# Optimization experiments

Measured on AMD Instinct MI355X. Metric: run time of the kernel, lower is better.

The kernel has to match this reference:

```python
import jax, jax.numpy as jnp
import numpy as np
from jax import lax

EPS = 1e-10
ALPHA = 1000.0

def _gauss_kernel(k=3, mu=0.0, sigma=3.0):
    g1 = np.linspace(-1.0, 1.0, k)
    x, y = np.meshgrid(g1, g1)
    d = np.sqrt(x ** 2 + y ** 2)
    g = np.exp(-(d - mu) ** 2 / (2.0 * sigma ** 2)) / (2.0 * np.pi * sigma ** 2)
    return jnp.asarray(g / g.sum(), jnp.float32)

def _sobel_kernel(k=3, transpose=False):
    r = np.linspace(-(k // 2), k // 2, k)
    x, y = np.meshgrid(r, r)
    den = x ** 2 + y ** 2
    den[:, k // 2] = 1.0
    s = x / den
    if transpose:
        s = s.T
    return jnp.asarray(s, jnp.float32)

def _canny_nms_kernels():
    # 8 directional difference kernels (center minus neighbor), E, SE, S, SW, W, NW, N, NE
    off = [(1, 2), (2, 2), (2, 1), (2, 0), (1, 0), (0, 0), (0, 1), (0, 2)]
    k = np.zeros((8, 3, 3), np.float32)
    k[:, 1, 1] = 1.0
    for i, (r, c) in enumerate(off):
        k[i, r, c] = -1.0
    return jnp.asarray(k)

def _dwconv_reflect(x, k2d):
    # depthwise 3x3 conv with reflect padding (same as padding_mode='reflect', groups=C)
    C = x.shape[1]
    xp = jnp.pad(x, ((0, 0), (0, 0), (1, 1), (1, 1)), mode='reflect')
    w = jnp.broadcast_to(k2d[None, None], (C, 1, 3, 3))
    return lax.conv_general_dilated(xp, w, (1, 1), 'VALID', feature_group_count=C)

def _forward(x, w_expand, w_perm_gauss, w_perm_sx, w_perm_sy, w_merge, low_t, high_t):
    gauss = _gauss_kernel(3, 0.0, 3.0)
    sob_x = _sobel_kernel(3, transpose=False)
    sob_y = _sobel_kernel(3, transpose=True)
    canny = _canny_nms_kernels()  # (8,3,3)
    # 1x1 channel expansion
    h = jnp.einsum('oc,bchw->bohw', w_expand, x)
    # gaussian blur (depthwise) + trainable 1x1 permute
    g = jnp.einsum('oc,bchw->bohw', w_perm_gauss, _dwconv_reflect(h, gauss))
    gx = jnp.einsum('oc,bchw->bohw', w_perm_sx, _dwconv_reflect(g, sob_x))
    gy = jnp.einsum('oc,bchw->bohw', w_perm_sy, _dwconv_reflect(g, sob_y))
    mag = jnp.sqrt(gx * gx + gy * gy + EPS)  # (B,C,H,W)
    # NMSConv2d: every output kernel applies the same directional diff summed over ALL input
    # channels, so the 8C outputs repeat with period 8 -> compute 8 dirs on the channel-sum.
    s = jnp.sum(mag, axis=1, keepdims=True)  # (B,1,H,W)
    dirs = lax.conv_general_dilated(s, canny[:, None], (1, 1), [(1, 1), (1, 1)])  # (B,8,H,W)
    deg = jnp.arctan2(gy, gx) * (180.0 / np.pi)
    idx = jnp.mod(jnp.round(deg / 45.0), 8.0).astype(jnp.int32)  # (B,C,H,W) in [0,8)
    pos = jnp.take_along_axis(dirs[:, None], idx[:, :, None], axis=2)[:, :, 0]
    neg = jnp.take_along_axis(dirs[:, None], ((idx + 4) % 8)[:, :, None], axis=2)[:, :, 0]
    nms = mag * ((pos > 0) & (neg > 0)).astype(mag.dtype)
    # soft double threshold (steep sigmoids)
    strong = jax.nn.sigmoid(ALPHA * (nms - high_t))
    weak = 0.5 * (jax.nn.sigmoid(ALPHA * (high_t - nms)) - jax.nn.sigmoid(ALPHA * (low_t - nms)))
    thr = weak + strong
    # merge C -> 1
    m = jnp.einsum('oc,bchw->bohw', w_merge, thr)  # (B,1,H,W)
    # one-step hysteresis: strong pixels promote neighbouring weak (==0.5) pixels
    img_strong = jnp.where(m == 1.0, m, 0.0)
    masked = (m == 0.5)
    hyst = _dwconv_reflect(img_strong, jnp.full((3, 3), 1.25, m.dtype))
    changed = jnp.where((hyst > 1.0) & masked, m, 0.0) + img_strong
    return changed

def setup_inputs() -> dict:
    key = jax.random.key(0)
    k0, k1, k2 = jax.random.split(key, 3)
    B, Cin, C, H, W = 8, 3, 8, 512, 512
    x = jax.random.uniform(k0, (B, Cin, H, W), jnp.float32)
    w_expand = jax.nn.softmax(jax.random.uniform(k1, (C, Cin), jnp.float32), axis=0)
    eye = jnp.eye(C, dtype=jnp.float32)
    bound = 1.0 / np.sqrt(C)
    w_merge = jax.random.uniform(k2, (1, C), jnp.float32, minval=-bound, maxval=bound)
    low_t = jnp.full((C, 1, 1), 0.1, jnp.float32)
    high_t = jnp.full((C, 1, 1), 0.2, jnp.float32)
    return {'x': x, 'w_expand': w_expand, 'w_perm_gauss': eye, 'w_perm_sx': eye,
            'w_perm_sy': eye, 'w_merge': w_merge, 'low_t': low_t, 'high_t': high_t}

def reference(x, w_expand, w_perm_gauss, w_perm_sx, w_perm_sy, w_merge, low_t, high_t):
    return _forward(x, w_expand, w_perm_gauss, w_perm_sx, w_perm_sy, w_merge, low_t, high_t)
```

## Files before the change

kernel.cpp:

```cpp
#include <hip/hip_runtime.h>
#include <math.h>

#define Bsz 8
#define HWp (512*512)
#define TS 32
#define SG 36
#define MG 34
#define XW 40
#define BW 38
#define NT 512
#define K2E 1442.6950408889634f
#define T2q 0.17157287525380993f

typedef float f2 __attribute__((ext_vector_type(2)));

#if __has_builtin(__builtin_amdgcn_exp2f)
#define EXP2F(x) __builtin_amdgcn_exp2f(x)
#else
#define EXP2F(x) __expf(0.6931471805599453f*(x))
#endif

__device__ __forceinline__ int refl(int i, int n) {
    i = (i < 0) ? -i : i;
    return (i >= n) ? (2*n - 2 - i) : i;
}

__global__ void k_mats(const float* __restrict__ we, const float* __restrict__ pg,
                       const float* __restrict__ psx, const float* __restrict__ psy,
                       const float* __restrict__ wm, const float* __restrict__ lowt,
                       const float* __restrict__ hight, float* __restrict__ mats) {
    if (threadIdx.x == 0 && blockIdx.x == 0) {
        float M1[8][3];
        for (int o = 0; o < 8; ++o)
            for (int c = 0; c < 3; ++c) {
                float a = 0.f;
                for (int k = 0; k < 8; ++k) a += pg[o*8+k] * we[k*3+c];
                M1[o][c] = a;
            }
        for (int o = 0; o < 8; ++o)
            for (int c = 0; c < 3; ++c) {
                float a = 0.f, b = 0.f;
                for (int k = 0; k < 8; ++k) { a += psx[o*8+k]*M1[k][c]; b += psy[o*8+k]*M1[k][c]; }
                mats[o*3+c]      = a;
                mats[24 + o*3+c] = b;
            }
        for (int o = 0; o < 8; ++o) {
            mats[48+o] = hight[o] * K2E;
            mats[56+o] = lowt[o]  * K2E;
            mats[64+o] = 0.5f * wm[o];
        }
        for (int j = 0; j < 4; ++j)
            for (int k = 0; k < 3; ++k)
                for (int e = 0; e < 2; ++e) {
                    mats[72  + (j*3+k)*2 + e] = mats[(2*j+e)*3 + k];
                    mats[120 + (j*3+k)*2 + e] = mats[24 + (2*j+e)*3 + k];
                }
    }
}

__global__ __launch_bounds__(NT) void k_fused(
    const float* __restrict__ x, const float* __restrict__ mats,
    float* __restrict__ out, float wc, float wE, float wk)
{
    __shared__ float sm1[3*XW*XW];
    __shared__ float blb[3*BW*BW];
    __shared__ int anyS;

    const int b  = blockIdx.z;
    const int x0 = blockIdx.x*TS, y0 = blockIdx.y*TS;
    const int t  = threadIdx.x;
    const bool inter = (blockIdx.x > 0) && ((int)blockIdx.x < (int)gridDim.x-1) &&
                       (blockIdx.y > 0) && ((int)blockIdx.y < (int)gridDim.y-1);

    if (t == 0) anyS = 0;

    const float* xb = x + (size_t)b*3*HWp;

    if (inter) {
        const float* xo = xb + (size_t)(y0-4)*512 + (x0-4);
        for (int i = t; i < 3*XW*10; i += NT) {
            int c = i/400; int j = i - c*400; int r = j/10; int q = j - r*10;
            float4 v = *(const float4*)(xo + (size_t)c*HWp + r*512 + q*4);
            *(float4*)&sm1[c*(XW*XW) + r*XW + q*4] = v;
        }
    } else {
        for (int i = t; i < XW*XW; i += NT) {
            int r = i/XW, cc = i - r*XW;
            size_t off = (size_t)refl(y0-4+r,512)*512 + refl(x0-4+cc,512);
            #pragma unroll
            for (int c = 0; c < 3; ++c)
                sm1[c*(XW*XW)+i] = xb[(size_t)c*HWp + off];
        }
    }
    __syncthreads();

    if (inter) {
        if (t < 494) {
            int g = t/38, cb = t - g*38, r0 = 3*g;
            #pragma unroll
            for (int c = 0; c < 3; ++c) {
                const float* col = &sm1[c*(XW*XW) + cb];
                float* bo = &blb[c*(BW*BW) + cb];
                float a0 = col[r0*XW],     a1 = col[r0*XW+1],     a2 = col[r0*XW+2];
                float e0 = col[(r0+1)*XW], e1 = col[(r0+1)*XW+1], e2 = col[(r0+1)*XW+2];
                #pragma unroll
                for (int ir = 0; ir < 3; ++ir) {
                    int r = r0 + ir;
                    if (r < BW) {
                        float f0 = col[(r+2)*XW], f1 = col[(r+2)*XW+1], f2v = col[(r+2)*XW+2];
                        float t0 = a0+f0, t1 = a1+f1, t2 = a2+f2v;
                        float u = t0+t2, v = e0+e2, w = t1+v;
                        bo[r*BW] = wk*u + wE*w + wc*e1;
                        a0=e0; a1=e1; a2=e2; e0=f0; e1=f1; e2=f2v;
                    }
                }
            }
        }
    } else {
        for (int i = t; i < BW*BW; i += NT) {
            int r = i/BW, cc = i - r*BW;
            int iy = refl(y0-3+r,512) - (y0-4);
            int ix = refl(x0-3+cc,512) - (x0-4);
            const int base = iy*XW + ix;
            #pragma unroll
            for (int c = 0; c < 3; ++c) {
                const float* xp = &sm1[c*(XW*XW) + base];
                blb[c*(BW*BW)+i] =
                    wk*(xp[-XW-1]+xp[-XW+1]+xp[XW-1]+xp[XW+1]) +
                    wE*(xp[-XW]+xp[-1]+xp[1]+xp[XW]) + wc*xp[0];
            }
        }
    }
    __syncthreads();

    float mg[3][8];
    unsigned qk[3];
    const int gC = t/36, csC = t - gC*36, r0C = 3*gC;
    const bool actC = (t < 432);
    if (actC) {
        float txv[3][3], tyv[3][3];
        #pragma unroll
        for (int c = 0; c < 3; ++c) {
            const float* blc = &blb[c*(BW*BW) + csC];
            float p0 = blc[r0C*BW],     p1 = blc[r0C*BW+1],     p2 = blc[r0C*BW+2];
            float q0 = blc[(r0C+1)*BW], q1 = blc[(r0C+1)*BW+1], q2 = blc[(r0C+1)*BW+2];
            float D0 = p2-p0, E0 = fmaf(0.5f, p0+p2, p1);
            float D1 = q2-q0, E1 = fmaf(0.5f, q0+q2, q1);
            #pragma unroll
            for (int ir = 0; ir < 3; ++ir) {
                const float* wr = &blc[(r0C+2+ir)*BW];
                float w0 = wr[0], w1 = wr[1], w2 = wr[2];
                float D2 = w2-w0, E2 = fmaf(0.5f, w0+w2, w1);
                txv[ir][c] = fmaf(0.5f, D0+D2, D1);
                tyv[ir][c] = E2 - E0;
                D0 = D1; D1 = D2; E0 = E1; E1 = E2;
            }
        }
        const f2* A2 = (const f2*)(mats + 72);
        const f2* B2 = (const f2*)(mats + 120);
        #pragma unroll
        for (int ir = 0; ir < 3; ++ir) {
            f2 s2 = {0.f, 0.f};
            unsigned pk = 0;
            #pragma unroll
            for (int j = 0; j < 4; ++j) {
                f2 gx = A2[j*3+0]*txv[ir][0] + A2[j*3+1]*txv[ir][1] + A2[j*3+2]*txv[ir][2];
                f2 gy = B2[j*3+0]*tyv[ir][0] + B2[j*3+1]*tyv[ir][1] + B2[j*3+2]*tyv[ir][2];
                f2 gx2 = gx*gx, gy2 = gy*gy;
                f2 r2 = gx2 + gy2 + (f2){1e-10f, 1e-10f};
                float m0 = __builtin_amdgcn_sqrtf(r2.x);
                float m1 = __builtin_amdgcn_sqrtf(r2.y);
                mg[ir][2*j] = m0; mg[ir][2*j+1] = m1;
                s2 += (f2){m0, m1};
                unsigned d0 = 1u | (((__float_as_uint(gx.x) ^ __float_as_uint(gy.x)) >> 30) & 2u);
                unsigned q0 = (gx2.x <= T2q*gy2.x) ? 2u : d0;
                q0 = (gy2.x <= T2q*gx2.x) ? 0u : q0;
                unsigned d1 = 1u | (((__float_as_uint(gx.y) ^ __float_as_uint(gy.y)) >> 30) & 2u);
                unsigned q1 = (gx2.y <= T2q*gy2.y) ? 2u : d1;
                q1 = (gy2.y <= T2q*gx2.y) ? 0u : q1;
                pk |= (q0 << (4*j)) | (q1 << (4*j+2));
            }
            qk[ir] = pk;
            #pragma unroll
            for (int o = 0; o < 8; ++o) { asm volatile("" : "+v"(mg[ir][o])); }
            asm volatile("" : "+v"(qk[ir]));
            int rr = r0C + ir;
            int gy_ = y0-2+rr, gx_ = x0-2+csC;
            bool inimg = ((unsigned)gy_ < 512u) && ((unsigned)gx_ < 512u);
            sm1[rr*SG + csC] = inimg ? (s2.x + s2.y) : 0.f;
        }
    }
    __syncthreads();

    bool anyL = false;
    {
        const float* sS = sm1;
        float* mS = sm1 + SG*SG;
        const f2* hiK2 = (const f2*)(mats + 48);
        const f2* loK2 = (const f2*)(mats + 56);
        const f2* wm2  = (const f2*)(mats + 64);
        if (actC && csC >= 1 && csC <= 34) {
            int ra = r0C-1 < 0 ? 0 : r0C-1;
            int rb = r0C;
            int rc = r0C+1;
            const float* pa = &sS[ra*SG + csC];
            const float* pb = &sS[rb*SG + csC];
            const float* pc = &sS[rc*SG + csC];
            float l0=pa[-1], c0=pa[0], r0v=pa[1];
            float l1=pb[-1], c1=pb[0], r1v=pb[1];
            float l2=pc[-1], c2=pc[0], r2v=pc[1];
            #pragma unroll
            for (int ir = 0; ir < 3; ++ir) {
                int r = r0C + ir;
                if (r >= 1 && r <= 34) {
                    float sc = c1;
                    unsigned mask = 0;
                    mask |= ((sc > r1v) && (sc > l1)) ? 1u : 0u;
                    mask |= ((sc > r2v) && (sc > l0)) ? 2u : 0u;
                    mask |= ((sc > c2)  && (sc > c0)) ? 4u : 0u;
                    mask |= ((sc > l2)  && (sc > r0v)) ? 8u : 0u;
                    unsigned pk = qk[ir];
                    f2 acc = {0.f, 0.f};
                    #pragma unroll
                    for (int j = 0; j < 4; ++j) {
                        unsigned ii = pk >> (4*j);
                        f2 nms;
                        nms.x = ((mask >> (ii & 3u)) & 1u)      ? mg[ir][2*j]   : 0.f;
                        nms.y = ((mask >> ((ii>>2) & 3u)) & 1u) ? mg[ir][2*j+1] : 0.f;
                        f2 aH = nms * (f2){-K2E,-K2E} + hiK2[j];
                        f2 aL = nms * (f2){-K2E,-K2E} + loK2[j];
                        f2 sh = { __builtin_amdgcn_rcpf(1.f + EXP2F(aH.x)),
                                  __builtin_amdgcn_rcpf(1.f + EXP2F(aH.y)) };
                        f2 sl = { __builtin_amdgcn_rcpf(1.f + EXP2F(aL.x)),
                                  __builtin_amdgcn_rcpf(1.f + EXP2F(aL.y)) };
                        acc += wm2[j]*(sh + sl);
                    }
                    float m = acc.x + acc.y;
                    mS[(r-1)*MG + (csC-1)] = m;
                    anyL |= (m == 1.0f);
                }
                if (ir < 2) {
                    int rn = r0C + 2 + ir; rn = rn > 35 ? 35 : rn;
                    const float* pn = &sS[rn*SG + csC];
                    l0=l1; c0=c1; r0v=r1v;
                    l1=l2; c1=c2; r1v=r2v;
                    l2=pn[-1]; c2=pn[0]; r2v=pn[1];
                }
            }
        }
    }
    if (anyL) anyS = 1;
    __syncthreads();

    {
        const float* mS = sm1 + SG*SG;
        float* op = out + (size_t)b*HWp;
        if (anyS == 0) {
            if (t < 256) {
                int row = t >> 3, q = t & 7;
                float4 z = {0.f, 0.f, 0.f, 0.f};
                *(float4*)(op + (size_t)(y0+row)*512 + x0 + q*4) = z;
            }
        } else {
            for (int i2 = t; i2 < TS*TS; i2 += NT) {
                int ty_ = i2>>5, tx_ = i2&31;
                int y = y0 + ty_, xg = x0 + tx_;
                const float* mp = &mS[(ty_+1)*MG + (tx_+1)];
                float mc = mp[0];
                float hy = 0.f;
                if (inter) {
                    #pragma unroll
                    for (int dy = -1; dy <= 1; ++dy)
                        #pragma unroll
                        for (int dx = -1; dx <= 1; ++dx)
                            hy += (mp[dy*MG+dx] == 1.0f) ? 1.25f : 0.f;
                } else {
                    #pragma unroll
                    for (int dy = -1; dy <= 1; ++dy)
                        #pragma unroll
                        for (int dx = -1; dx <= 1; ++dx) {
                            int ly = refl(y+dy,512) - (y0-1);
                            int lx = refl(xg+dx,512) - (x0-1);
                            hy += (mS[ly*MG+lx] == 1.0f) ? 1.25f : 0.f;
                        }
                }
                float strong = (mc == 1.0f) ? mc : 0.f;
                op[(size_t)y*512 + xg] =
                    (((hy > 1.0f) && (mc == 0.5f)) ? mc : 0.f) + strong;
            }
        }
    }
}

extern "C" void kernel_launch(void* const* d_in, const int* in_sizes, int n_in,
                              void* d_out, int out_size, void* d_ws, size_t ws_size,
                              hipStream_t stream) {
    const float* x    = (const float*)d_in[0];
    const float* we   = (const float*)d_in[1];
    const float* pg   = (const float*)d_in[2];
    const float* psx  = (const float*)d_in[3];
    const float* psy  = (const float*)d_in[4];
    const float* wm   = (const float*)d_in[5];
    const float* lowt = (const float*)d_in[6];
    const float* hit  = (const float*)d_in[7];
    float* mats = (float*)d_ws;
    float* outp = (float*)d_out;

    double e1 = exp(-1.0/18.0), e2 = exp(-2.0/18.0);
    double sum = 1.0 + 4.0*e1 + 4.0*e2;
    float wc = (float)(1.0/sum), wE = (float)(e1/sum), wk = (float)(e2/sum);

    k_mats<<<1, 64, 0, stream>>>(we, pg, psx, psy, wm, lowt, hit, mats);
    k_fused<<<dim3(512/TS, 512/TS, Bsz), dim3(NT), 0, stream>>>(
        x, mats, outp, wc, wE, wk);
}
```

Measured before the change: 52.17 us.

## Widen tiles to 64x32 with 1024 threads and fold weight prep into fused kernel

Changes the tile from 32x32 to 64x32 with 1024 threads per block, which shrinks the relative halo overhead for loads and the blur/gradient stages. Removes the separate single-thread k_mats launch. Each block now computes the combined channel matrices in shared memory and reads them as wave-uniform values via readfirstlane. Larger blocks and more shared memory per block may lower occupancy, and every block redoes the small matrix computation.

```diff
diff --git a/kernel.cpp b/kernel.cpp
--- a/kernel.cpp
+++ b/kernel.cpp
@@ -3,12 +3,17 @@
 
 #define Bsz 8
 #define HWp (512*512)
-#define TS 32
-#define SG 36
-#define MG 34
-#define XW 40
-#define BW 38
-#define NT 512
+#define TSX 64
+#define TSY 32
+#define XR 40
+#define XC 72
+#define BR 38
+#define BC 70
+#define SR 36
+#define SC 68
+#define MR 34
+#define MC 66
+#define NT 1024
 #define K2E 1442.6950408889634f
 #define T2q 0.17157287525380993f
 
@@ -24,154 +29,170 @@
     i = (i < 0) ? -i : i;
     return (i >= n) ? (2*n - 2 - i) : i;
 }
-
-__global__ void k_mats(const float* __restrict__ we, const float* __restrict__ pg,
-                       const float* __restrict__ psx, const float* __restrict__ psy,
-                       const float* __restrict__ wm, const float* __restrict__ lowt,
-                       const float* __restrict__ hight, float* __restrict__ mats) {
-    if (threadIdx.x == 0 && blockIdx.x == 0) {
-        float M1[8][3];
-        for (int o = 0; o < 8; ++o)
-            for (int c = 0; c < 3; ++c) {
-                float a = 0.f;
-                for (int k = 0; k < 8; ++k) a += pg[o*8+k] * we[k*3+c];
-                M1[o][c] = a;
-            }
-        for (int o = 0; o < 8; ++o)
-            for (int c = 0; c < 3; ++c) {
-                float a = 0.f, b = 0.f;
-                for (int k = 0; k < 8; ++k) { a += psx[o*8+k]*M1[k][c]; b += psy[o*8+k]*M1[k][c]; }
-                mats[o*3+c]      = a;
-                mats[24 + o*3+c] = b;
-            }
-        for (int o = 0; o < 8; ++o) {
-            mats[48+o] = hight[o] * K2E;
-            mats[56+o] = lowt[o]  * K2E;
-            mats[64+o] = 0.5f * wm[o];
-        }
-        for (int j = 0; j < 4; ++j)
-            for (int k = 0; k < 3; ++k)
-                for (int e = 0; e < 2; ++e) {
-                    mats[72  + (j*3+k)*2 + e] = mats[(2*j+e)*3 + k];
-                    mats[120 + (j*3+k)*2 + e] = mats[24 + (2*j+e)*3 + k];
-                }
-    }
-}
-
-__global__ __launch_bounds__(NT) void k_fused(
-    const float* __restrict__ x, const float* __restrict__ mats,
+__device__ __forceinline__ float ldsUf(float v) {
+    return __uint_as_float(__builtin_amdgcn_readfirstlane(__float_as_uint(v)));
+}
+__device__ __forceinline__ f2 ldsU2(const float* p) {
+    f2 v = *(const f2*)p;
+    f2 r; r.x = ldsUf(v.x); r.y = ldsUf(v.y);
+    return r;
+}
+__device__ __forceinline__ f2 splat(float v) { f2 r = {v, v}; return r; }
+
+__global__ __launch_bounds__(NT, 4) void k_fused(
+    const float* __restrict__ x,
+    const float* __restrict__ we, const float* __restrict__ pg,
+    const float* __restrict__ psx, const float* __restrict__ psy,
+    const float* __restrict__ wm, const float* __restrict__ lowt,
+    const float* __restrict__ hight,
     float* __restrict__ out, float wc, float wE, float wk)
 {
-    __shared__ float sm1[3*XW*XW];
-    __shared__ float blb[3*BW*BW];
+    __shared__ __align__(16) float xw[3*XR*XC];
+    __shared__ __align__(16) float blb[3*BR*BC];
+    __shared__ __align__(16) float matsL[168];
     __shared__ int anyS;
 
     const int b  = blockIdx.z;
-    const int x0 = blockIdx.x*TS, y0 = blockIdx.y*TS;
+    const int x0 = blockIdx.x*TSX, y0 = blockIdx.y*TSY;
     const int t  = threadIdx.x;
     const bool inter = (blockIdx.x > 0) && ((int)blockIdx.x < (int)gridDim.x-1) &&
                        (blockIdx.y > 0) && ((int)blockIdx.y < (int)gridDim.y-1);
 
     if (t == 0) anyS = 0;
 
+    if (t < 24) {
+        int o = t/3, c = t - o*3;
+        float a = 0.f;
+        #pragma unroll
+        for (int k = 0; k < 8; ++k) a = fmaf(pg[o*8+k], we[k*3+c], a);
+        matsL[144 + t] = a;
+        float av = 0.f, bv = 0.f;
+        #pragma unroll
+        for (int k = 0; k < 8; ++k) {
+            float m1 = matsL[144 + k*3 + c];
+            av = fmaf(psx[o*8+k], m1, av);
+            bv = fmaf(psy[o*8+k], m1, bv);
+        }
+        matsL[t]      = av;
+        matsL[24 + t] = bv;
+        int pi = ((o>>1)*3 + c)*2 + (o&1);
+        matsL[72  + pi] = av;
+        matsL[120 + pi] = bv;
+    } else if (t < 32) {
+        int o = t - 24;
+        matsL[48+o] = hight[o] * K2E;
+        matsL[56+o] = lowt[o]  * K2E;
+        matsL[64+o] = 0.5f * wm[o];
+    }
+
     const float* xb = x + (size_t)b*3*HWp;
 
     if (inter) {
         const float* xo = xb + (size_t)(y0-4)*512 + (x0-4);
-        for (int i = t; i < 3*XW*10; i += NT) {
-            int c = i/400; int j = i - c*400; int r = j/10; int q = j - r*10;
+        for (int i = t; i < 3*XR*18; i += NT) {
+            int c = i/720; int j = i - c*720; int r = j/18; int q = j - r*18;
             float4 v = *(const float4*)(xo + (size_t)c*HWp + r*512 + q*4);
-            *(float4*)&sm1[c*(XW*XW) + r*XW + q*4] = v;
+            *(float4*)&xw[c*(XR*XC) + r*XC + q*4] = v;
         }
     } else {
-        for (int i = t; i < XW*XW; i += NT) {
-            int r = i/XW, cc = i - r*XW;
+        for (int i = t; i < XR*XC; i += NT) {
+            int r = i/XC, cc = i - r*XC;
             size_t off = (size_t)refl(y0-4+r,512)*512 + refl(x0-4+cc,512);
             #pragma unroll
             for (int c = 0; c < 3; ++c)
-                sm1[c*(XW*XW)+i] = xb[(size_t)c*HWp + off];
+                xw[c*(XR*XC)+i] = xb[(size_t)c*HWp + off];
         }
     }
     __syncthreads();
 
     if (inter) {
-        if (t < 494) {
-            int g = t/38, cb = t - g*38, r0 = 3*g;
+        if (t < 13*BC) {
+            int g = t/BC, cb = t - g*BC, r0 = 3*g;
             #pragma unroll
             for (int c = 0; c < 3; ++c) {
-                const float* col = &sm1[c*(XW*XW) + cb];
-                float* bo = &blb[c*(BW*BW) + cb];
-                float a0 = col[r0*XW],     a1 = col[r0*XW+1],     a2 = col[r0*XW+2];
-                float e0 = col[(r0+1)*XW], e1 = col[(r0+1)*XW+1], e2 = col[(r0+1)*XW+2];
+                const float* col = &xw[c*(XR*XC) + cb];
+                float* bo = &blb[c*(BR*BC) + cb];
+                float a0 = col[r0*XC],     a1 = col[r0*XC+1],     a2 = col[r0*XC+2];
+                float e0 = col[(r0+1)*XC], e1 = col[(r0+1)*XC+1], e2 = col[(r0+1)*XC+2];
                 #pragma unroll
                 for (int ir = 0; ir < 3; ++ir) {
                     int r = r0 + ir;
-                    if (r < BW) {
-                        float f0 = col[(r+2)*XW], f1 = col[(r+2)*XW+1], f2v = col[(r+2)*XW+2];
+                    if (r < BR) {
+                        float f0 = col[(r+2)*XC], f1 = col[(r+2)*XC+1], f2v = col[(r+2)*XC+2];
                         float t0 = a0+f0, t1 = a1+f1, t2 = a2+f2v;
                         float u = t0+t2, v = e0+e2, w = t1+v;
-                        bo[r*BW] = wk*u + wE*w + wc*e1;
+                        bo[r*BC] = wk*u + wE*w + wc*e1;
                         a0=e0; a1=e1; a2=e2; e0=f0; e1=f1; e2=f2v;
                     }
                 }
             }
         }
     } else {
-        for (int i = t; i < BW*BW; i += NT) {
-            int r = i/BW, cc = i - r*BW;
+        for (int i = t; i < BR*BC; i += NT) {
+            int r = i/BC, cc = i - r*BC;
             int iy = refl(y0-3+r,512) - (y0-4);
             int ix = refl(x0-3+cc,512) - (x0-4);
-            const int base = iy*XW + ix;
+            const int base = iy*XC + ix;
             #pragma unroll
             for (int c = 0; c < 3; ++c) {
-                const float* xp = &sm1[c*(XW*XW) + base];
-                blb[c*(BW*BW)+i] =
-                    wk*(xp[-XW-1]+xp[-XW+1]+xp[XW-1]+xp[XW+1]) +
-                    wE*(xp[-XW]+xp[-1]+xp[1]+xp[XW]) + wc*xp[0];
+                const float* xp = &xw[c*(XR*XC) + base];
+                blb[c*(BR*BC)+i] =
+                    wk*(xp[-XC-1]+xp[-XC+1]+xp[XC-1]+xp[XC+1]) +
+                    wE*(xp[-XC]+xp[-1]+xp[1]+xp[XC]) + wc*xp[0];
             }
         }
     }
     __syncthreads();
 
-    float mg[3][8];
+    f2 mg2[3][4];
     unsigned qk[3];
-    const int gC = t/36, csC = t - gC*36, r0C = 3*gC;
-    const bool actC = (t < 432);
+    const int gC = t/SC, csC = t - gC*SC, r0C = 3*gC;
+    const bool actC = (t < 12*SC);
     if (actC) {
-        float txv[3][3], tyv[3][3];
+        f2 A2[12], B2[12];
+        #pragma unroll
+        for (int j = 0; j < 12; ++j) {
+            A2[j] = ldsU2(matsL + 72  + 2*j);
+            B2[j] = ldsU2(matsL + 120 + 2*j);
+        }
+        float D0[3], D1[3], E0[3], E1[3];
         #pragma unroll
         for (int c = 0; c < 3; ++c) {
-            const float* blc = &blb[c*(BW*BW) + csC];
-            float p0 = blc[r0C*BW],     p1 = blc[r0C*BW+1],     p2 = blc[r0C*BW+2];
-            float q0 = blc[(r0C+1)*BW], q1 = blc[(r0C+1)*BW+1], q2 = blc[(r0C+1)*BW+2];
-            float D0 = p2-p0, E0 = fmaf(0.5f, p0+p2, p1);
-            float D1 = q2-q0, E1 = fmaf(0.5f, q0+q2, q1);
-            #pragma unroll
-            for (int ir = 0; ir < 3; ++ir) {
-                const float* wr = &blc[(r0C+2+ir)*BW];
+            const float* blc = &blb[c*(BR*BC) + csC];
+            float p0 = blc[r0C*BC],     p1 = blc[r0C*BC+1],     p2 = blc[r0C*BC+2];
+            float q0 = blc[(r0C+1)*BC], q1 = blc[(r0C+1)*BC+1], q2 = blc[(r0C+1)*BC+2];
+            D0[c] = p2-p0; E0[c] = fmaf(0.5f, p0+p2, p1);
+            D1[c] = q2-q0; E1[c] = fmaf(0.5f, q0+q2, q1);
+        }
+        const f2 eps2 = {1e-10f, 1e-10f};
+        #pragma unroll
+        for (int ir = 0; ir < 3; ++ir) {
+            float txv[3], tyv[3];
+            #pragma unroll
+            for (int c = 0; c < 3; ++c) {
+                const float* wr = &blb[c*(BR*BC) + (r0C+2+ir)*BC + csC];
                 float w0 = wr[0], w1 = wr[1], w2 = wr[2];
                 float D2 = w2-w0, E2 = fmaf(0.5f, w0+w2, w1);
-                txv[ir][c] = fmaf(0.5f, D0+D2, D1);
-                tyv[ir][c] = E2 - E0;
-                D0 = D1; D1 = D2; E0 = E1; E1 = E2;
-            }
-        }
-        const f2* A2 = (const f2*)(mats + 72);
-        const f2* B2 = (const f2*)(mats + 120);
-        #pragma unroll
-        for (int ir = 0; ir < 3; ++ir) {
+                txv[c] = fmaf(0.5f, D0[c]+D2, D1[c]);
+                tyv[c] = E2 - E0[c];
+                D0[c] = D1[c]; D1[c] = D2; E0[c] = E1[c]; E1[c] = E2;
+            }
             f2 s2 = {0.f, 0.f};
             unsigned pk = 0;
             #pragma unroll
             for (int j = 0; j < 4; ++j) {
-                f2 gx = A2[j*3+0]*txv[ir][0] + A2[j*3+1]*txv[ir][1] + A2[j*3+2]*txv[ir][2];
-                f2 gy = B2[j*3+0]*tyv[ir][0] + B2[j*3+1]*tyv[ir][1] + B2[j*3+2]*tyv[ir][2];
+                f2 gx = __builtin_elementwise_fma(A2[j*3+0], splat(txv[0]),
+                        __builtin_elementwise_fma(A2[j*3+1], splat(txv[1]),
+                                                  A2[j*3+2]*splat(txv[2])));
+                f2 gy = __builtin_elementwise_fma(B2[j*3+0], splat(tyv[0]),
+                        __builtin_elementwise_fma(B2[j*3+1], splat(tyv[1]),
+                                                  B2[j*3+2]*splat(tyv[2])));
                 f2 gx2 = gx*gx, gy2 = gy*gy;
-                f2 r2 = gx2 + gy2 + (f2){1e-10f, 1e-10f};
-                float m0 = __builtin_amdgcn_sqrtf(r2.x);
-                float m1 = __builtin_amdgcn_sqrtf(r2.y);
-                mg[ir][2*j] = m0; mg[ir][2*j+1] = m1;
-                s2 += (f2){m0, m1};
+                f2 r2 = gx2 + gy2 + eps2;
+                f2 m; m.x = __builtin_amdgcn_sqrtf(r2.x);
+                      m.y = __builtin_amdgcn_sqrtf(r2.y);
+                mg2[ir][j] = m;
+                s2 += m;
                 unsigned d0 = 1u | (((__float_as_uint(gx.x) ^ __float_as_uint(gy.x)) >> 30) & 2u);
                 unsigned q0 = (gx2.x <= T2q*gy2.x) ? 2u : d0;
                 q0 = (gy2.x <= T2q*gx2.x) ? 0u : q0;
@@ -182,37 +203,40 @@
             }
             qk[ir] = pk;
             #pragma unroll
-            for (int o = 0; o < 8; ++o) { asm volatile("" : "+v"(mg[ir][o])); }
+            for (int j = 0; j < 4; ++j) { asm volatile("" : "+v"(mg2[ir][j])); }
             asm volatile("" : "+v"(qk[ir]));
             int rr = r0C + ir;
             int gy_ = y0-2+rr, gx_ = x0-2+csC;
             bool inimg = ((unsigned)gy_ < 512u) && ((unsigned)gx_ < 512u);
-            sm1[rr*SG + csC] = inimg ? (s2.x + s2.y) : 0.f;
+            xw[rr*SC + csC] = inimg ? (s2.x + s2.y) : 0.f;
         }
     }
     __syncthreads();
 
     bool anyL = false;
     {
-        const float* sS = sm1;
-        float* mS = sm1 + SG*SG;
-        const f2* hiK2 = (const f2*)(mats + 48);
-        const f2* loK2 = (const f2*)(mats + 56);
-        const f2* wm2  = (const f2*)(mats + 64);
-        if (actC && csC >= 1 && csC <= 34) {
+        const float* sS = xw;
+        float* mS = xw + SR*SC;
+        if (actC && csC >= 1 && csC <= MC) {
+            f2 hiK2[4], loK2[4], wm2[4];
+            #pragma unroll
+            for (int j = 0; j < 4; ++j) {
+                hiK2[j] = ldsU2(matsL + 48 + 2*j);
+                loK2[j] = ldsU2(matsL + 56 + 2*j);
+                wm2[j]  = ldsU2(matsL + 64 + 2*j);
+            }
             int ra = r0C-1 < 0 ? 0 : r0C-1;
-            int rb = r0C;
-            int rc = r0C+1;
-            const float* pa = &sS[ra*SG + csC];
-            const float* pb = &sS[rb*SG + csC];
-            const float* pc = &sS[rc*SG + csC];
+            const float* pa = &sS[ra*SC + csC];
+            const float* pb = &sS[r0C*SC + csC];
+            const float* pc = &sS[(r0C+1)*SC + csC];
             float l0=pa[-1], c0=pa[0], r0v=pa[1];
             float l1=pb[-1], c1=pb[0], r1v=pb[1];
             float l2=pc[-1], c2=pc[0], r2v=pc[1];
+            const f2 nK2E = {-K2E, -K2E};
             #pragma unroll
             for (int ir = 0; ir < 3; ++ir) {
                 int r = r0C + ir;
-                if (r >= 1 && r <= 34) {
+                if (r >= 1 && r <= MR) {
                     float sc = c1;
                     unsigned mask = 0;
                     mask |= ((sc > r1v) && (sc > l1)) ? 1u : 0u;
@@ -225,23 +249,23 @@
                     for (int j = 0; j < 4; ++j) {
                         unsigned ii = pk >> (4*j);
                         f2 nms;
-                        nms.x = ((mask >> (ii & 3u)) & 1u)      ? mg[ir][2*j]   : 0.f;
-                        nms.y = ((mask >> ((ii>>2) & 3u)) & 1u) ? mg[ir][2*j+1] : 0.f;
-                        f2 aH = nms * (f2){-K2E,-K2E} + hiK2[j];
-                        f2 aL = nms * (f2){-K2E,-K2E} + loK2[j];
-                        f2 sh = { __builtin_amdgcn_rcpf(1.f + EXP2F(aH.x)),
-                                  __builtin_amdgcn_rcpf(1.f + EXP2F(aH.y)) };
-                        f2 sl = { __builtin_amdgcn_rcpf(1.f + EXP2F(aL.x)),
-                                  __builtin_amdgcn_rcpf(1.f + EXP2F(aL.y)) };
-                        acc += wm2[j]*(sh + sl);
+                        nms.x = ((mask >> (ii & 3u)) & 1u)      ? mg2[ir][j].x : 0.f;
+                        nms.y = ((mask >> ((ii>>2) & 3u)) & 1u) ? mg2[ir][j].y : 0.f;
+                        f2 aH = __builtin_elementwise_fma(nms, nK2E, hiK2[j]);
+                        f2 aL = __builtin_elementwise_fma(nms, nK2E, loK2[j]);
+                        f2 sh; sh.x = __builtin_amdgcn_rcpf(1.f + EXP2F(aH.x));
+                               sh.y = __builtin_amdgcn_rcpf(1.f + EXP2F(aH.y));
+                        f2 sl; sl.x = __builtin_amdgcn_rcpf(1.f + EXP2F(aL.x));
+                               sl.y = __builtin_amdgcn_rcpf(1.f + EXP2F(aL.y));
+                        acc = __builtin_elementwise_fma(wm2[j], sh + sl, acc);
                     }
                     float m = acc.x + acc.y;
-                    mS[(r-1)*MG + (csC-1)] = m;
+                    mS[(r-1)*MC + (csC-1)] = m;
                     anyL |= (m == 1.0f);
                 }
                 if (ir < 2) {
-                    int rn = r0C + 2 + ir; rn = rn > 35 ? 35 : rn;
-                    const float* pn = &sS[rn*SG + csC];
+                    int rn = r0C + 2 + ir; rn = rn > SR-1 ? SR-1 : rn;
+                    const float* pn = &sS[rn*SC + csC];
                     l0=l1; c0=c1; r0v=r1v;
                     l1=l2; c1=c2; r1v=r2v;
                     l2=pn[-1]; c2=pn[0]; r2v=pn[1];
@@ -253,19 +277,19 @@
     __syncthreads();
 
     {
-        const float* mS = sm1 + SG*SG;
+        const float* mS = xw + SR*SC;
         float* op = out + (size_t)b*HWp;
         if (anyS == 0) {
-            if (t < 256) {
-                int row = t >> 3, q = t & 7;
+            if (t < 512) {
+                int row = t >> 4, q = t & 15;
                 float4 z = {0.f, 0.f, 0.f, 0.f};
                 *(float4*)(op + (size_t)(y0+row)*512 + x0 + q*4) = z;
             }
         } else {
-            for (int i2 = t; i2 < TS*TS; i2 += NT) {
-                int ty_ = i2>>5, tx_ = i2&31;
+            for (int i2 = t; i2 < TSY*TSX; i2 += NT) {
+                int ty_ = i2>>6, tx_ = i2&63;
                 int y = y0 + ty_, xg = x0 + tx_;
-                const float* mp = &mS[(ty_+1)*MG + (tx_+1)];
+                const float* mp = &mS[(ty_+1)*MC + (tx_+1)];
                 float mc = mp[0];
                 float hy = 0.f;
                 if (inter) {
@@ -273,7 +297,7 @@
                     for (int dy = -1; dy <= 1; ++dy)
                         #pragma unroll
                         for (int dx = -1; dx <= 1; ++dx)
-                            hy += (mp[dy*MG+dx] == 1.0f) ? 1.25f : 0.f;
+                            hy += (mp[dy*MC+dx] == 1.0f) ? 1.25f : 0.f;
                 } else {
                     #pragma unroll
                     for (int dy = -1; dy <= 1; ++dy)
@@ -281,7 +305,7 @@
                         for (int dx = -1; dx <= 1; ++dx) {
                             int ly = refl(y+dy,512) - (y0-1);
                             int lx = refl(xg+dx,512) - (x0-1);
-                            hy += (mS[ly*MG+lx] == 1.0f) ? 1.25f : 0.f;
+                            hy += (mS[ly*MC+lx] == 1.0f) ? 1.25f : 0.f;
                         }
                 }
                 float strong = (mc == 1.0f) ? mc : 0.f;
@@ -303,14 +327,12 @@
     const float* wm   = (const float*)d_in[5];
     const float* lowt = (const float*)d_in[6];
     const float* hit  = (const float*)d_in[7];
-    float* mats = (float*)d_ws;
     float* outp = (float*)d_out;
 
     double e1 = exp(-1.0/18.0), e2 = exp(-2.0/18.0);
     double sum = 1.0 + 4.0*e1 + 4.0*e2;
     float wc = (float)(1.0/sum), wE = (float)(e1/sum), wk = (float)(e2/sum);
 
-    k_mats<<<1, 64, 0, stream>>>(we, pg, psx, psy, wm, lowt, hit, mats);
-    k_fused<<<dim3(512/TS, 512/TS, Bsz), dim3(NT), 0, stream>>>(
-        x, mats, outp, wc, wE, wk);
-}
+    k_fused<<<dim3(512/TSX, 512/TSY, Bsz), dim3(NT), 0, stream>>>(
+        x, we, pg, psx, psy, wm, lowt, hit, outp, wc, wE, wk);
+}
```

Result: slower. 54.52 us (+4.5%).

## Fold weight-prep kernel into fused kernel and share one exp between sigmoids

Applied to the files above, without the earlier changes.

Removes the separate single-thread k_mats launch: each block now computes the combined channel matrices and threshold constants into shared memory, then broadcasts them to scalar registers with readfirstlane. Both threshold sigmoids are rewritten to use a single exp2 per value, scaled by precomputed exp2(±d) factors, which halves the transcendental count. The Sobel loop is also reordered to interleave per-row work. The cost is that every block repeats the small matrix computation and a few global loads.

```diff
diff --git a/kernel.cpp b/kernel.cpp
--- a/kernel.cpp
+++ b/kernel.cpp
@@ -24,46 +24,26 @@
     i = (i < 0) ? -i : i;
     return (i >= n) ? (2*n - 2 - i) : i;
 }
-
-__global__ void k_mats(const float* __restrict__ we, const float* __restrict__ pg,
-                       const float* __restrict__ psx, const float* __restrict__ psy,
-                       const float* __restrict__ wm, const float* __restrict__ lowt,
-                       const float* __restrict__ hight, float* __restrict__ mats) {
-    if (threadIdx.x == 0 && blockIdx.x == 0) {
-        float M1[8][3];
-        for (int o = 0; o < 8; ++o)
-            for (int c = 0; c < 3; ++c) {
-                float a = 0.f;
-                for (int k = 0; k < 8; ++k) a += pg[o*8+k] * we[k*3+c];
-                M1[o][c] = a;
-            }
-        for (int o = 0; o < 8; ++o)
-            for (int c = 0; c < 3; ++c) {
-                float a = 0.f, b = 0.f;
-                for (int k = 0; k < 8; ++k) { a += psx[o*8+k]*M1[k][c]; b += psy[o*8+k]*M1[k][c]; }
-                mats[o*3+c]      = a;
-                mats[24 + o*3+c] = b;
-            }
-        for (int o = 0; o < 8; ++o) {
-            mats[48+o] = hight[o] * K2E;
-            mats[56+o] = lowt[o]  * K2E;
-            mats[64+o] = 0.5f * wm[o];
-        }
-        for (int j = 0; j < 4; ++j)
-            for (int k = 0; k < 3; ++k)
-                for (int e = 0; e < 2; ++e) {
-                    mats[72  + (j*3+k)*2 + e] = mats[(2*j+e)*3 + k];
-                    mats[120 + (j*3+k)*2 + e] = mats[24 + (2*j+e)*3 + k];
-                }
-    }
+__device__ __forceinline__ float ldsUf(float v) {
+    return __uint_as_float(__builtin_amdgcn_readfirstlane(__float_as_uint(v)));
+}
+__device__ __forceinline__ f2 ldsU2(const float* p) {
+    f2 v = *(const f2*)p;
+    f2 r; r.x = ldsUf(v.x); r.y = ldsUf(v.y);
+    return r;
 }
 
 __global__ __launch_bounds__(NT) void k_fused(
-    const float* __restrict__ x, const float* __restrict__ mats,
+    const float* __restrict__ x,
+    const float* __restrict__ we, const float* __restrict__ pg,
+    const float* __restrict__ psx, const float* __restrict__ psy,
+    const float* __restrict__ wm, const float* __restrict__ lowt,
+    const float* __restrict__ hight,
     float* __restrict__ out, float wc, float wE, float wk)
 {
     __shared__ float sm1[3*XW*XW];
     __shared__ float blb[3*BW*BW];
+    __shared__ __align__(16) float matsL[104];
     __shared__ int anyS;
 
     const int b  = blockIdx.z;
@@ -73,6 +53,32 @@
                        (blockIdx.y > 0) && ((int)blockIdx.y < (int)gridDim.y-1);
 
     if (t == 0) anyS = 0;
+
+    if (t < 24) {
+        int o = t/3, c = t - o*3;
+        float a = 0.f;
+        #pragma unroll
+        for (int k = 0; k < 8; ++k) a = fmaf(pg[o*8+k], we[k*3+c], a);
+        matsL[80 + t] = a;
+        float av = 0.f, bv = 0.f;
+        #pragma unroll
+        for (int k = 0; k < 8; ++k) {
+            float m1 = matsL[80 + k*3 + c];
+            av = fmaf(psx[o*8+k], m1, av);
+            bv = fmaf(psy[o*8+k], m1, bv);
+        }
+        int pi = ((o>>1)*3 + c)*2 + (o&1);
+        matsL[pi]      = av;
+        matsL[24 + pi] = bv;
+    } else if (t < 32) {
+        int o = t - 24;
+        float hi = hight[o], lo = lowt[o];
+        float d = K2E * 0.5f * (hi - lo);
+        matsL[48+o] = K2E * 0.5f * (hi + lo);
+        matsL[56+o] = exp2f(d);
+        matsL[64+o] = exp2f(-d);
+        matsL[72+o] = 0.5f * wm[o];
+    }
 
     const float* xb = x + (size_t)b*3*HWp;
 
@@ -133,61 +139,69 @@
     }
     __syncthreads();
 
-    float mg[3][8];
+    f2 mg2[3][4];
     unsigned qk[3];
     const int gC = t/36, csC = t - gC*36, r0C = 3*gC;
     const bool actC = (t < 432);
     if (actC) {
-        float txv[3][3], tyv[3][3];
+        f2 A2[12], B2[12];
+        #pragma unroll
+        for (int j = 0; j < 12; ++j) {
+            A2[j] = ldsU2(matsL + 2*j);
+            B2[j] = ldsU2(matsL + 24 + 2*j);
+        }
+        float D0[3], D1[3], E0[3], E1[3];
         #pragma unroll
         for (int c = 0; c < 3; ++c) {
             const float* blc = &blb[c*(BW*BW) + csC];
             float p0 = blc[r0C*BW],     p1 = blc[r0C*BW+1],     p2 = blc[r0C*BW+2];
             float q0 = blc[(r0C+1)*BW], q1 = blc[(r0C+1)*BW+1], q2 = blc[(r0C+1)*BW+2];
-            float D0 = p2-p0, E0 = fmaf(0.5f, p0+p2, p1);
-            float D1 = q2-q0, E1 = fmaf(0.5f, q0+q2, q1);
-            #pragma unroll
-            for (int ir = 0; ir < 3; ++ir) {
-                const float* wr = &blc[(r0C+2+ir)*BW];
+            D0[c] = p2-p0; E0[c] = fmaf(0.5f, p0+p2, p1);
+            D1[c] = q2-q0; E1[c] = fmaf(0.5f, q0+q2, q1);
+        }
+        #pragma unroll
+        for (int ir = 0; ir < 3; ++ir) {
+            float txv[3], tyv[3];
+            #pragma unroll
+            for (int c = 0; c < 3; ++c) {
+                const float* wr = &blb[c*(BW*BW) + (r0C+2+ir)*BW + csC];
                 float w0 = wr[0], w1 = wr[1], w2 = wr[2];
                 float D2 = w2-w0, E2 = fmaf(0.5f, w0+w2, w1);
-                txv[ir][c] = fmaf(0.5f, D0+D2, D1);
-                tyv[ir][c] = E2 - E0;
-                D0 = D1; D1 = D2; E0 = E1; E1 = E2;
-            }
-        }
-        const f2* A2 = (const f2*)(mats + 72);
-        const f2* B2 = (const f2*)(mats + 120);
-        #pragma unroll
-        for (int ir = 0; ir < 3; ++ir) {
-            f2 s2 = {0.f, 0.f};
+                txv[c] = fmaf(0.5f, D0[c]+D2, D1[c]);
+                tyv[c] = E2 - E0[c];
+                D0[c] = D1[c]; D1[c] = D2; E0[c] = E1[c]; E1[c] = E2;
+            }
+            float s = 0.f;
             unsigned pk = 0;
             #pragma unroll
             for (int j = 0; j < 4; ++j) {
-                f2 gx = A2[j*3+0]*txv[ir][0] + A2[j*3+1]*txv[ir][1] + A2[j*3+2]*txv[ir][2];
-                f2 gy = B2[j*3+0]*tyv[ir][0] + B2[j*3+1]*tyv[ir][1] + B2[j*3+2]*tyv[ir][2];
-                f2 gx2 = gx*gx, gy2 = gy*gy;
-                f2 r2 = gx2 + gy2 + (f2){1e-10f, 1e-10f};
-                float m0 = __builtin_amdgcn_sqrtf(r2.x);
-                float m1 = __builtin_amdgcn_sqrtf(r2.y);
-                mg[ir][2*j] = m0; mg[ir][2*j+1] = m1;
-                s2 += (f2){m0, m1};
-                unsigned d0 = 1u | (((__float_as_uint(gx.x) ^ __float_as_uint(gy.x)) >> 30) & 2u);
-                unsigned q0 = (gx2.x <= T2q*gy2.x) ? 2u : d0;
-                q0 = (gy2.x <= T2q*gx2.x) ? 0u : q0;
-                unsigned d1 = 1u | (((__float_as_uint(gx.y) ^ __float_as_uint(gy.y)) >> 30) & 2u);
-                unsigned q1 = (gx2.y <= T2q*gy2.y) ? 2u : d1;
-                q1 = (gy2.y <= T2q*gx2.y) ? 0u : q1;
+                float gxa = fmaf(A2[j*3].x, txv[0], fmaf(A2[j*3+1].x, txv[1], A2[j*3+2].x*txv[2]));
+                float gxb = fmaf(A2[j*3].y, txv[0], fmaf(A2[j*3+1].y, txv[1], A2[j*3+2].y*txv[2]));
+                float gya = fmaf(B2[j*3].x, tyv[0], fmaf(B2[j*3+1].x, tyv[1], B2[j*3+2].x*tyv[2]));
+                float gyb = fmaf(B2[j*3].y, tyv[0], fmaf(B2[j*3+1].y, tyv[1], B2[j*3+2].y*tyv[2]));
+                float gx2a = gxa*gxa, gy2a = gya*gya;
+                float gx2b = gxb*gxb, gy2b = gyb*gyb;
+                f2 m;
+                m.x = __builtin_amdgcn_sqrtf(gx2a + gy2a + 1e-10f);
+                m.y = __builtin_amdgcn_sqrtf(gx2b + gy2b + 1e-10f);
+                mg2[ir][j] = m;
+                s += m.x + m.y;
+                unsigned d0 = 1u | (((__float_as_uint(gxa) ^ __float_as_uint(gya)) >> 30) & 2u);
+                unsigned q0 = (gx2a <= T2q*gy2a) ? 2u : d0;
+                q0 = (gy2a <= T2q*gx2a) ? 0u : q0;
+                unsigned d1 = 1u | (((__float_as_uint(gxb) ^ __float_as_uint(gyb)) >> 30) & 2u);
+                unsigned q1 = (gx2b <= T2q*gy2b) ? 2u : d1;
+                q1 = (gy2b <= T2q*gx2b) ? 0u : q1;
                 pk |= (q0 << (4*j)) | (q1 << (4*j+2));
             }
             qk[ir] = pk;
             #pragma unroll
-            for (int o = 0; o < 8; ++o) { asm volatile("" : "+v"(mg[ir][o])); }
+            for (int j = 0; j < 4; ++j) { asm volatile("" : "+v"(mg2[ir][j])); }
             asm volatile("" : "+v"(qk[ir]));
             int rr = r0C + ir;
             int gy_ = y0-2+rr, gx_ = x0-2+csC;
             bool inimg = ((unsigned)gy_ < 512u) && ((unsigned)gx_ < 512u);
-            sm1[rr*SG + csC] = inimg ? (s2.x + s2.y) : 0.f;
+            sm1[rr*SG + csC] = inimg ? s : 0.f;
         }
     }
     __syncthreads();
@@ -196,16 +210,19 @@
     {
         const float* sS = sm1;
         float* mS = sm1 + SG*SG;
-        const f2* hiK2 = (const f2*)(mats + 48);
-        const f2* loK2 = (const f2*)(mats + 56);
-        const f2* wm2  = (const f2*)(mats + 64);
         if (actC && csC >= 1 && csC <= 34) {
+            f2 mid2[4], ph2[4], pl2[4], wm2[4];
+            #pragma unroll
+            for (int j = 0; j < 4; ++j) {
+                mid2[j] = ldsU2(matsL + 48 + 2*j);
+                ph2[j]  = ldsU2(matsL + 56 + 2*j);
+                pl2[j]  = ldsU2(matsL + 64 + 2*j);
+                wm2[j]  = ldsU2(matsL + 72 + 2*j);
+            }
             int ra = r0C-1 < 0 ? 0 : r0C-1;
-            int rb = r0C;
-            int rc = r0C+1;
             const float* pa = &sS[ra*SG + csC];
-            const float* pb = &sS[rb*SG + csC];
-            const float* pc = &sS[rc*SG + csC];
+            const float* pb = &sS[r0C*SG + csC];
+            const float* pc = &sS[(r0C+1)*SG + csC];
             float l0=pa[-1], c0=pa[0], r0v=pa[1];
             float l1=pb[-1], c1=pb[0], r1v=pb[1];
             float l2=pc[-1], c2=pc[0], r2v=pc[1];
@@ -220,22 +237,21 @@
                     mask |= ((sc > c2)  && (sc > c0)) ? 4u : 0u;
                     mask |= ((sc > l2)  && (sc > r0v)) ? 8u : 0u;
                     unsigned pk = qk[ir];
-                    f2 acc = {0.f, 0.f};
+                    float m = 0.f;
                     #pragma unroll
                     for (int j = 0; j < 4; ++j) {
                         unsigned ii = pk >> (4*j);
-                        f2 nms;
-                        nms.x = ((mask >> (ii & 3u)) & 1u)      ? mg[ir][2*j]   : 0.f;
-                        nms.y = ((mask >> ((ii>>2) & 3u)) & 1u) ? mg[ir][2*j+1] : 0.f;
-                        f2 aH = nms * (f2){-K2E,-K2E} + hiK2[j];
-                        f2 aL = nms * (f2){-K2E,-K2E} + loK2[j];
-                        f2 sh = { __builtin_amdgcn_rcpf(1.f + EXP2F(aH.x)),
-                                  __builtin_amdgcn_rcpf(1.f + EXP2F(aH.y)) };
-                        f2 sl = { __builtin_amdgcn_rcpf(1.f + EXP2F(aL.x)),
-                                  __builtin_amdgcn_rcpf(1.f + EXP2F(aL.y)) };
-                        acc += wm2[j]*(sh + sl);
+                        float n0 = ((mask >> (ii & 3u)) & 1u)      ? mg2[ir][j].x : 0.f;
+                        float n1 = ((mask >> ((ii>>2) & 3u)) & 1u) ? mg2[ir][j].y : 0.f;
+                        float e0 = EXP2F(fmaf(n0, -K2E, mid2[j].x));
+                        float e1 = EXP2F(fmaf(n1, -K2E, mid2[j].y));
+                        float sh0 = __builtin_amdgcn_rcpf(fmaf(e0, ph2[j].x, 1.f));
+                        float sl0 = __builtin_amdgcn_rcpf(fmaf(e0, pl2[j].x, 1.f));
+                        float sh1 = __builtin_amdgcn_rcpf(fmaf(e1, ph2[j].y, 1.f));
+                        float sl1 = __builtin_amdgcn_rcpf(fmaf(e1, pl2[j].y, 1.f));
+                        m = fmaf(wm2[j].x, sh0 + sl0, m);
+                        m = fmaf(wm2[j].y, sh1 + sl1, m);
                     }
-                    float m = acc.x + acc.y;
                     mS[(r-1)*MG + (csC-1)] = m;
                     anyL |= (m == 1.0f);
                 }
@@ -303,14 +319,12 @@
     const float* wm   = (const float*)d_in[5];
     const float* lowt = (const float*)d_in[6];
     const float* hit  = (const float*)d_in[7];
-    float* mats = (float*)d_ws;
     float* outp = (float*)d_out;
 
     double e1 = exp(-1.0/18.0), e2 = exp(-2.0/18.0);
     double sum = 1.0 + 4.0*e1 + 4.0*e2;
     float wc = (float)(1.0/sum), wE = (float)(e1/sum), wk = (float)(e2/sum);
 
-    k_mats<<<1, 64, 0, stream>>>(we, pg, psx, psy, wm, lowt, hit, mats);
     k_fused<<<dim3(512/TS, 512/TS, Bsz), dim3(NT), 0, stream>>>(
-        x, mats, outp, wc, wE, wk);
-}
+        x, we, pg, psx, psy, wm, lowt, hit, outp, wc, wE, wk);
+}
```

Measured after the change: 46.24 us. -11.4%, faster.
